# Optimization experiments

Hardware: AMD Instinct MI355X
Metric: run time of the kernel (lower is better)

The kernel has to match this reference:

```python
import jax, jax.numpy as jnp
import numpy as np

H = 16
N_TASKS, N_DATA, N_DEV = 400_000, 200_000, 8


def _edges(key, n_src, n_dst, e):
    k1, k2 = jax.random.split(key)
    src = jax.random.randint(k1, (e,), 0, n_src)
    dst = jax.random.randint(k2, (e,), 0, n_dst)
    return jnp.stack([src, dst]).astype(jnp.int64)


def setup_inputs() -> dict:
    key = jax.random.key(0)
    ks = jax.random.split(key, 16)
    inp = {
        "x_tasks": jax.random.normal(ks[0], (N_TASKS, 12), jnp.float32),
        "x_data": jax.random.normal(ks[1], (N_DATA, 5), jnp.float32),
        "x_devices": jax.random.normal(ks[2], (N_DEV, 12), jnp.float32),
        "ei_data_tasks": _edges(ks[3], N_DATA, N_TASKS, 1_600_000),
        "ei_tasks_data": _edges(ks[4], N_TASKS, N_DATA, 1_600_000),
        "ei_tasks_devices": _edges(ks[5], N_TASKS, N_DEV, 400_000),
        "ei_devices_tasks": _edges(ks[6], N_DEV, N_TASKS, 400_000),
        "ei_data_devices": _edges(ks[7], N_DATA, N_DEV, 200_000),
        "ei_devices_data": _edges(ks[8], N_DEV, N_DATA, 200_000),
        "ei_tt_to": _edges(ks[9], N_TASKS, N_TASKS, 800_000),
        "ei_tt_from": _edges(ks[10], N_TASKS, N_TASKS, 800_000),
        # stacked GraphConv weights, grouped by input dim
        # W_rel5:  [0]=data->tasks, [1]=data->devices
        "W_rel5": jax.random.normal(ks[11], (2, 5, H), jnp.float32) * 0.3,
        # W_rel12: [0]=tasks->data,[1]=tasks->devices,[2]=devices->tasks,[3]=devices->data,[4]=tt_to,[5]=tt_from
        "W_rel12": jax.random.normal(ks[12], (6, 12, H), jnp.float32) * 0.2,
        # b_rel order: dt_t, t_d, t_dev, dev_t, d_dev, dev_d, tt_to, tt_from
        "b_rel": jax.random.normal(ks[13], (8, H), jnp.float32) * 0.1,
        # W_root5: [0]=tasks->data (dst data), [1]=devices->data
        "W_root5": jax.random.normal(ks[14], (2, 5, H), jnp.float32) * 0.3,
        # W_root12: [0]=data->tasks,[1]=tasks->devices,[2]=devices->tasks,[3]=data->devices,[4]=tt_to,[5]=tt_from
        "W_root12": jax.random.normal(ks[15], (6, 12, H), jnp.float32) * 0.2,
        # LayerNorm params: [0]=tasks, [1]=data, [2]=devices
        "ln_gamma": jnp.ones((3, H), jnp.float32),
        "ln_beta": jnp.zeros((3, H), jnp.float32),
    }
    return inp


def _graph_conv(x_src, x_dst, ei, W_rel, b_rel, W_root):
    # PyG GraphConv(aggr='add'): lin_rel(scatter_add(x_src[src] -> dst)) + lin_root(x_dst)
    agg = jax.ops.segment_sum(x_src[ei[0]], ei[1], num_segments=x_dst.shape[0])
    return agg @ W_rel + b_rel + x_dst @ W_root


def _layer_norm(x, gamma, beta, eps=1e-5):
    mu = jnp.mean(x, axis=-1, keepdims=True)
    var = jnp.mean(jnp.square(x - mu), axis=-1, keepdims=True)
    return (x - mu) * jax.lax.rsqrt(var + eps) * gamma + beta


def reference(x_tasks, x_data, x_devices,
              ei_data_tasks, ei_tasks_data, ei_tasks_devices, ei_devices_tasks,
              ei_data_devices, ei_devices_data, ei_tt_to, ei_tt_from,
              W_rel5, W_rel12, b_rel, W_root5, W_root12, ln_gamma, ln_beta):
    # HeteroConv(aggr='sum'): sum relation outputs per destination node type
    tasks = (
        _graph_conv(x_data, x_tasks, ei_data_tasks, W_rel5[0], b_rel[0], W_root12[0])
        + _graph_conv(x_devices, x_tasks, ei_devices_tasks, W_rel12[2], b_rel[3], W_root12[2])
        + _graph_conv(x_tasks, x_tasks, ei_tt_to, W_rel12[4], b_rel[6], W_root12[4])
        + _graph_conv(x_tasks, x_tasks, ei_tt_from, W_rel12[5], b_rel[7], W_root12[5])
    )
    data = (
        _graph_conv(x_tasks, x_data, ei_tasks_data, W_rel12[0], b_rel[1], W_root5[0])
        + _graph_conv(x_devices, x_data, ei_devices_data, W_rel12[3], b_rel[5], W_root5[1])
    )
    devices = (
        _graph_conv(x_tasks, x_devices, ei_tasks_devices, W_rel12[1], b_rel[2], W_root12[1])
        + _graph_conv(x_data, x_devices, ei_data_devices, W_rel5[1], b_rel[4], W_root12[3])
    )
    slope = 0.01
    tasks = jax.nn.leaky_relu(_layer_norm(tasks, ln_gamma[0], ln_beta[0]), slope)
    data = jax.nn.leaky_relu(_layer_norm(data, ln_gamma[1], ln_beta[1]), slope)
    devices = jax.nn.leaky_relu(_layer_norm(devices, ln_gamma[2], ln_beta[2]), slope)
    return tasks, data, devices
```

## Files before the change

kernel.cpp:

```cpp
#include <hip/hip_runtime.h>
#include <hip/hip_fp16.h>

#define LRELU(v) ((v) >= 0.0f ? (v) : 0.01f * (v))
#define EPB 8192
#define SHIFT 7
#define PAIRS 1600

struct PartDesc {
    const int* src; const int* dst;
    unsigned* part; int* cursor;
    int E, B, cap, chunk0;
    unsigned tag;
};

struct PrepArgs {
    PartDesc r[6];
    int part_end;
    const int *tdev_e; int E_tdev; int sd12_b0, sd12_nb;
    const int *ddev_e; int E_ddev; int sd5_b0, sd5_nb;
    const float *x_tasks, *x_data, *x_dev;
    float *aggT_dev, *aggD_dev;
    __half *h_tasks; int NT; int ct_b0;
    __half *h_data;  int ND; int cd_b0;
};

template<int F>
__device__ __forceinline__ void loadrow(const float* __restrict__ x, unsigned s, float* v) {
    const float* p = x + (size_t)s * F;
    #pragma unroll
    for (int f = 0; f < F; ++f) v[f] = p[f];
}
template<>
__device__ __forceinline__ void loadrow<12>(const float* __restrict__ x, unsigned s, float* v) {
    const float4* p = (const float4*)(x + (size_t)s * 12);
    float4 a = p[0], b = p[1], c = p[2];
    v[0]=a.x; v[1]=a.y; v[2]=a.z; v[3]=a.w;
    v[4]=b.x; v[5]=b.y; v[6]=b.z; v[7]=b.w;
    v[8]=c.x; v[9]=c.y; v[10]=c.z; v[11]=c.w;
}

template<int F>
__device__ void scatter_dev_body(const float* __restrict__ x, const int* __restrict__ src,
                                 const int* __restrict__ dst, int E,
                                 float* __restrict__ agg, float* s_agg,
                                 int bl, int nb, int t)
{
    for (int i = t; i < 8 * F; i += 256) s_agg[i] = 0.0f;
    __syncthreads();
    const int stride = nb * 256;
    for (int e = bl * 256 + t; e < E; e += stride) {
        float v[F];
        loadrow<F>(x, (unsigned)src[e], v);
        int d = dst[e];
        #pragma unroll
        for (int f = 0; f < F; ++f) atomicAdd(&s_agg[d * F + f], v[f]);
    }
    __syncthreads();
    if (t < 8 * F) atomicAdd(&agg[t], s_agg[t]);
}

__global__ __launch_bounds__(256)
void prep_k(PrepArgs A)
{
    __shared__ unsigned shp[2 * PAIRS];
    const int bid = blockIdx.x;
    const int t = threadIdx.x;

    if (bid < A.part_end) {
        unsigned* hist = shp;
        unsigned* base = shp + PAIRS;
        int ri = 0;
        #pragma unroll
        for (int k = 1; k < 6; ++k) if (bid >= A.r[k].chunk0) ri = k;
        const PartDesc d = A.r[ri];
        const int e0 = (bid - d.chunk0) * EPB;
        const int e1 = min(d.E, e0 + EPB);
        const int npair = (d.B + 1) >> 1;

        for (int i = t; i < npair; i += 256) hist[i] = 0u;
        __syncthreads();
        for (int e = e0 + t; e < e1; e += 256) {
            int b = d.dst[e] >> SHIFT;
            atomicAdd(&hist[b >> 1], 1u << ((b & 1) << 4));
        }
        __syncthreads();
        for (int i = t; i < npair; i += 256) {
            unsigned h = hist[i];
            unsigned lo = h & 0xffffu, hi = h >> 16;
            unsigned blo = lo ? (unsigned)atomicAdd(&d.cursor[2 * i],     (int)lo) : 0u;
            unsigned bhi = hi ? (unsigned)atomicAdd(&d.cursor[2 * i + 1], (int)hi) : 0u;
            base[i] = (blo & 0xffffu) | (bhi << 16);
            hist[i] = 0u;
        }
        __syncthreads();
        for (int e = e0 + t; e < e1; e += 256) {
            int dd = d.dst[e];
            int b = dd >> SHIFT;
            unsigned s16 = (unsigned)(b & 1) << 4;
            unsigned r = atomicAdd(&hist[b >> 1], 1u << s16);
            unsigned idx = ((r >> s16) & 0xffffu) + ((base[b >> 1] >> s16) & 0xffffu);
            if ((int)idx < d.cap)
                d.part[(size_t)b * d.cap + idx] =
                    ((unsigned)d.src[e] << 9) | (((unsigned)dd & 127u) << 2) | d.tag;
        }
    } else if (bid < A.sd5_b0) {
        scatter_dev_body<12>(A.x_tasks, A.tdev_e, A.tdev_e + A.E_tdev, A.E_tdev,
                             A.aggT_dev, (float*)shp, bid - A.sd12_b0, A.sd12_nb, t);
    } else if (bid < A.ct_b0) {
        scatter_dev_body<5>(A.x_data, A.ddev_e, A.ddev_e + A.E_ddev, A.E_ddev,
                            A.aggD_dev, (float*)shp, bid - A.sd5_b0, A.sd5_nb, t);
    } else if (bid < A.cd_b0) {
        int row = (bid - A.ct_b0) * 256 + t;
        if (row < A.NT) {
            const float* xr = A.x_tasks + (size_t)row * 12;
            __half h[16];
            #pragma unroll
            for (int j = 0; j < 12; ++j) h[j] = __float2half(xr[j]);
            #pragma unroll
            for (int j = 12; j < 16; ++j) h[j] = __half(0.0f);
            uint4* dst = (uint4*)(A.h_tasks + (size_t)row * 16);
            dst[0] = *(const uint4*)h;
            dst[1] = *(const uint4*)(h + 8);
        }
    } else {
        int row = (bid - A.cd_b0) * 256 + t;
        if (row < A.ND) {
            const float* xr = A.x_data + (size_t)row * 5;
            __half h[8];
            #pragma unroll
            for (int j = 0; j < 5; ++j) h[j] = __float2half(xr[j]);
            #pragma unroll
            for (int j = 5; j < 8; ++j) h[j] = __half(0.0f);
            *(uint4*)(A.h_data + (size_t)row * 8) = *(const uint4*)h;
        }
    }
}

struct FusedArgs {
    const unsigned *p_task, *p_data;
    const int *c_task, *c_data;
    int cap_t, cap_d;
    const __half *h_tasks, *h_data;
    const float *x_dev, *x_tasks, *x_data;
    const float *aggT_dev, *aggD_dev;
    const float *W_rel5, *W_rel12, *b_rel, *W_root5, *W_root12, *ln_g, *ln_b;
    float *out_tasks, *out_data, *out_dev;
    int NT, ND, NDEV, Bt, Bd;
};

__device__ __forceinline__ void issue_task(unsigned e, const FusedArgs& A, uint4* r) {
    unsigned rel = e & 3u, s = e >> 9;
    if (rel == 0u) {
        r[0] = *(const uint4*)(A.h_data + (size_t)s * 8);
    } else if (rel == 1u) {
        const uint4* q = (const uint4*)(A.x_dev + (size_t)s * 12);
        r[0] = q[0]; r[1] = q[1]; r[2] = q[2];
    } else {
        const uint4* q = (const uint4*)(A.h_tasks + (size_t)s * 16);
        r[0] = q[0]; r[1] = q[1];
    }
}
__device__ __forceinline__ void commit_task(unsigned e, const uint4* r, float* acc) {
    unsigned rel = e & 3u;
    float* a = acc + ((e >> 2) & 127u) * 41;
    if (rel == 0u) {
        const __half2* h = (const __half2*)r;
        float2 f0 = __half22float2(h[0]), f1 = __half22float2(h[1]), f2 = __half22float2(h[2]);
        atomicAdd(a + 0, f0.x); atomicAdd(a + 1, f0.y);
        atomicAdd(a + 2, f1.x); atomicAdd(a + 3, f1.y);
        atomicAdd(a + 4, f2.x);
    } else if (rel == 1u) {
        const float* f = (const float*)r;
        #pragma unroll
        for (int j = 0; j < 12; ++j) atomicAdd(a + 5 + j, f[j]);
    } else {
        float* base = a + (rel == 2u ? 17 : 29);
        const __half2* h = (const __half2*)r;
        #pragma unroll
        for (int j = 0; j < 6; ++j) {
            float2 f = __half22float2(h[j]);
            atomicAdd(base + 2 * j,     f.x);
            atomicAdd(base + 2 * j + 1, f.y);
        }
    }
}

__device__ __forceinline__ void issue_data(unsigned e, const FusedArgs& A, uint4* r) {
    unsigned rel = e & 3u, s = e >> 9;
    if (rel == 0u) {
        const uint4* q = (const uint4*)(A.h_tasks + (size_t)s * 16);
        r[0] = q[0]; r[1] = q[1];
    } else {
        const uint4* q = (const uint4*)(A.x_dev + (size_t)s * 12);
        r[0] = q[0]; r[1] = q[1]; r[2] = q[2];
    }
}
__device__ __forceinline__ void commit_data(unsigned e, const uint4* r, float* acc) {
    unsigned rel = e & 3u;
    float* a = acc + ((e >> 2) & 127u) * 25;
    if (rel == 0u) {
        const __half2* h = (const __half2*)r;
        #pragma unroll
        for (int j = 0; j < 6; ++j) {
            float2 f = __half22float2(h[j]);
            atomicAdd(a + 2 * j,     f.x);
            atomicAdd(a + 2 * j + 1, f.y);
        }
    } else {
        const float* f = (const float*)r;
        #pragma unroll
        for (int j = 0; j < 12; ++j) atomicAdd(a + 12 + j, f[j]);
    }
}

__device__ __forceinline__
void ln_store(float* o, const float* __restrict__ sg, const float* __restrict__ sbt,
              float* __restrict__ op)
{
    float mu = 0.0f;
    #pragma unroll
    for (int k = 0; k < 16; ++k) mu += o[k];
    mu *= 0.0625f;
    float var = 0.0f;
    #pragma unroll
    for (int k = 0; k < 16; ++k) { float d = o[k] - mu; var = fmaf(d, d, var); }
    var *= 0.0625f;
    const float r = rsqrtf(var + 1e-5f);
    #pragma unroll
    for (int k = 0; k < 16; ++k) {
        float v = (o[k] - mu) * r * sg[k] + sbt[k];
        o[k] = LRELU(v);
    }
    float4* q = (float4*)op;
    const float4* s = (const float4*)o;
    q[0] = s[0]; q[1] = s[1]; q[2] = s[2]; q[3] = s[3];
}

__global__ __launch_bounds__(512, 8)
void fused_k(FusedArgs A)
{
    __shared__ __align__(16) float lds[6144];
    const int bid = blockIdx.x;
    const int t = threadIdx.x;

    if (bid < A.Bt) {
        float* acc = lds;
        float* sW  = lds + 5248;
        float* sb  = lds + 6096;
        float* sg  = lds + 6112;
        float* sbt = lds + 6128;

        for (int i = t; i < 5248; i += 512) acc[i] = 0.0f;
        for (int i = t; i < 80; i += 512) sW[i] = A.W_rel5[i];
        for (int i = t; i < 192; i += 512) {
            sW[80  + i] = A.W_rel12[384 + i];
            sW[272 + i] = A.W_rel12[768 + i];
            sW[464 + i] = A.W_rel12[960 + i];
            sW[656 + i] = A.W_root12[i] + A.W_root12[384 + i]
                        + A.W_root12[768 + i] + A.W_root12[960 + i];
        }
        if (t < 16) {
            sb[t]  = A.b_rel[t] + A.b_rel[48 + t] + A.b_rel[96 + t] + A.b_rel[112 + t];
            sg[t]  = A.ln_g[t];
            sbt[t] = A.ln_b[t];
        }
        __syncthreads();

        const unsigned* p = A.p_task + (size_t)bid * A.cap_t;
        const int cnt = min(A.c_task[bid], A.cap_t);
        int i = t;
        for (; i + 512 < cnt; i += 1024) {
            unsigned e0 = p[i], e1 = p[i + 512];
            uint4 r0[3], r1[3];
            issue_task(e0, A, r0);
            issue_task(e1, A, r1);
            commit_task(e0, r0, acc);
            commit_task(e1, r1, acc);
        }
        if (i < cnt) {
            unsigned e = p[i];
            uint4 r[3];
            issue_task(e, A, r);
            commit_task(e, r, acc);
        }
        __syncthreads();

        const int node = t >> 2, part = t & 3;
        const int row = (bid << SHIFT) + node;
        if (row < A.NT) {
            const float* ar = acc + node * 41;
            const int p4 = part * 4;
            float o0 = sb[p4], o1 = sb[p4 + 1], o2 = sb[p4 + 2], o3 = sb[p4 + 3];
            #pragma unroll
            for (int f = 0; f < 41; ++f) {
                float v = ar[f];
                float4 w = *(const float4*)(sW + f * 16 + p4);
                o0 = fmaf(v, w.x, o0); o1 = fmaf(v, w.y, o1);
                o2 = fmaf(v, w.z, o2); o3 = fmaf(v, w.w, o3);
            }
            const float* xr = A.x_tasks + (size_t)row * 12;
            #pragma unroll
            for (int f = 0; f < 12; ++f) {
                float v = xr[f];
                float4 w = *(const float4*)(sW + (41 + f) * 16 + p4);
                o0 = fmaf(v, w.x, o0); o1 = fmaf(v, w.y, o1);
                o2 = fmaf(v, w.z, o2); o3 = fmaf(v, w.w, o3);
            }
            float s = o0 + o1 + o2 + o3;
            s += __shfl_xor(s, 1); s += __shfl_xor(s, 2);
            const float mu = s * 0.0625f;
            float d0 = o0 - mu, d1 = o1 - mu, d2 = o2 - mu, d3 = o3 - mu;
            float q = d0*d0 + d1*d1 + d2*d2 + d3*d3;
            q += __shfl_xor(q, 1); q += __shfl_xor(q, 2);
            const float r = rsqrtf(q * 0.0625f + 1e-5f);
            float4 out;
            out.x = LRELU(d0 * r * sg[p4]     + sbt[p4]);
            out.y = LRELU(d1 * r * sg[p4 + 1] + sbt[p4 + 1]);
            out.z = LRELU(d2 * r * sg[p4 + 2] + sbt[p4 + 2]);
            out.w = LRELU(d3 * r * sg[p4 + 3] + sbt[p4 + 3]);
            *(float4*)(A.out_tasks + (size_t)row * 16 + p4) = out;
        }
    } else if (bid < A.Bt + A.Bd) {
        float* acc = lds;
        float* sW  = lds + 3200;
        float* sb  = lds + 3664;
        float* sg  = lds + 3680;
        float* sbt = lds + 3696;

        for (int i = t; i < 3200; i += 512) acc[i] = 0.0f;
        for (int i = t; i < 192; i += 512) {
            sW[i]       = A.W_rel12[i];
            sW[192 + i] = A.W_rel12[576 + i];
        }
        for (int i = t; i < 80; i += 512)
            sW[384 + i] = A.W_root5[i] + A.W_root5[80 + i];
        if (t < 16) {
            sb[t]  = A.b_rel[16 + t] + A.b_rel[80 + t];
            sg[t]  = A.ln_g[16 + t];
            sbt[t] = A.ln_b[16 + t];
        }
        __syncthreads();

        const int b = bid - A.Bt;
        const unsigned* p = A.p_data + (size_t)b * A.cap_d;
        const int cnt = min(A.c_data[b], A.cap_d);
        int i = t;
        for (; i + 512 < cnt; i += 1024) {
            unsigned e0 = p[i], e1 = p[i + 512];
            uint4 r0[3], r1[3];
            issue_data(e0, A, r0);
            issue_data(e1, A, r1);
            commit_data(e0, r0, acc);
            commit_data(e1, r1, acc);
        }
        if (i < cnt) {
            unsigned e = p[i];
            uint4 r[3];
            issue_data(e, A, r);
            commit_data(e, r, acc);
        }
        __syncthreads();

        const int node = t >> 2, part = t & 3;
        const int row = (b << SHIFT) + node;
        if (row < A.ND) {
            const float* ar = acc + node * 25;
            const int p4 = part * 4;
            float o0 = sb[p4], o1 = sb[p4 + 1], o2 = sb[p4 + 2], o3 = sb[p4 + 3];
            #pragma unroll
            for (int f = 0; f < 24; ++f) {
                float v = ar[f];
                float4 w = *(const float4*)(sW + f * 16 + p4);
                o0 = fmaf(v, w.x, o0); o1 = fmaf(v, w.y, o1);
                o2 = fmaf(v, w.z, o2); o3 = fmaf(v, w.w, o3);
            }
            const float* xr = A.x_data + (size_t)row * 5;
            #pragma unroll
            for (int f = 0; f < 5; ++f) {
                float v = xr[f];
                float4 w = *(const float4*)(sW + (24 + f) * 16 + p4);
                o0 = fmaf(v, w.x, o0); o1 = fmaf(v, w.y, o1);
                o2 = fmaf(v, w.z, o2); o3 = fmaf(v, w.w, o3);
            }
            float s = o0 + o1 + o2 + o3;
            s += __shfl_xor(s, 1); s += __shfl_xor(s, 2);
            const float mu = s * 0.0625f;
            float d0 = o0 - mu, d1 = o1 - mu, d2 = o2 - mu, d3 = o3 - mu;
            float q = d0*d0 + d1*d1 + d2*d2 + d3*d3;
            q += __shfl_xor(q, 1); q += __shfl_xor(q, 2);
            const float r = rsqrtf(q * 0.0625f + 1e-5f);
            float4 out;
            out.x = LRELU(d0 * r * sg[p4]     + sbt[p4]);
            out.y = LRELU(d1 * r * sg[p4 + 1] + sbt[p4 + 1]);
            out.z = LRELU(d2 * r * sg[p4 + 2] + sbt[p4 + 2]);
            out.w = LRELU(d3 * r * sg[p4 + 3] + sbt[p4 + 3]);
            *(float4*)(A.out_data + (size_t)row * 16 + p4) = out;
        }
    } else {
        const int i = t;
        if (i < A.NDEV) {
            float o[16];
            #pragma unroll
            for (int k = 0; k < 16; ++k) o[k] = A.b_rel[32 + k] + A.b_rel[64 + k];
            #pragma unroll
            for (int j = 0; j < 12; ++j) {
                float fj = A.aggT_dev[i * 12 + j];
                #pragma unroll
                for (int k = 0; k < 16; ++k) o[k] = fmaf(fj, A.W_rel12[192 + j * 16 + k], o[k]);
            }
            #pragma unroll
            for (int j = 0; j < 5; ++j) {
                float fj = A.aggD_dev[i * 5 + j];
                #pragma unroll
                for (int k = 0; k < 16; ++k) o[k] = fmaf(fj, A.W_rel5[80 + j * 16 + k], o[k]);
            }
            #pragma unroll
            for (int j = 0; j < 12; ++j) {
                float fj = A.x_dev[i * 12 + j];
                #pragma unroll
                for (int k = 0; k < 16; ++k)
                    o[k] = fmaf(fj, A.W_root12[192 + j * 16 + k] + A.W_root12[576 + j * 16 + k], o[k]);
            }
            ln_store(o, A.ln_g + 32, A.ln_b + 32, A.out_dev + (size_t)i * 16);
        }
    }
}

extern "C" void kernel_launch(void* const* d_in, const int* in_sizes, int n_in,
                              void* d_out, int out_size, void* d_ws, size_t ws_size,
                              hipStream_t stream)
{
    const float* x_tasks = (const float*)d_in[0];
    const float* x_data  = (const float*)d_in[1];
    const float* x_dev   = (const float*)d_in[2];
    const int* ei_dt    = (const int*)d_in[3];
    const int* ei_td    = (const int*)d_in[4];
    const int* ei_tdev  = (const int*)d_in[5];
    const int* ei_devt  = (const int*)d_in[6];
    const int* ei_ddev  = (const int*)d_in[7];
    const int* ei_devd  = (const int*)d_in[8];
    const int* ei_to    = (const int*)d_in[9];
    const int* ei_from  = (const int*)d_in[10];
    const float* W_rel5   = (const float*)d_in[11];
    const float* W_rel12  = (const float*)d_in[12];
    const float* b_rel    = (const float*)d_in[13];
    const float* W_root5  = (const float*)d_in[14];
    const float* W_root12 = (const float*)d_in[15];
    const float* ln_g     = (const float*)d_in[16];
    const float* ln_b     = (const float*)d_in[17];

    const int NT   = in_sizes[0] / 12;
    const int ND   = in_sizes[1] / 5;
    const int NDEV = in_sizes[2] / 12;
    const int E_dt   = in_sizes[3]  / 2;
    const int E_td   = in_sizes[4]  / 2;
    const int E_tdev = in_sizes[5]  / 2;
    const int E_devt = in_sizes[6]  / 2;
    const int E_ddev = in_sizes[7]  / 2;
    const int E_devd = in_sizes[8]  / 2;
    const int E_to   = in_sizes[9]  / 2;
    const int E_from = in_sizes[10] / 2;

    const int B_t = (NT + 127) / 128;
    const int B_d = (ND + 127) / 128;

    auto capf = [](long long E, int B) {
        int mean = (int)(E / B) + 1;
        int c = mean + mean / 4 + 128;
        return (c + 3) & ~3;
    };
    const int cap_t = capf((long long)E_dt + E_devt + E_to + E_from, B_t);
    const int cap_d = capf((long long)E_td + E_devd, B_d);

    float* ws = (float*)d_ws;
    size_t o = 0;
    int* c_task = (int*)(ws + o); o += 3200;
    int* c_data = (int*)(ws + o); o += 1600;
    float* aggT_dev = ws + o; o += 96;
    float* aggD_dev = ws + o; o += 48;
    const size_t zero_bytes = o * sizeof(float);
    o = (o + 3) & ~(size_t)3;
    __half* h_tasks = (__half*)(ws + o); o += (size_t)NT * 8;
    __half* h_data  = (__half*)(ws + o); o += (size_t)ND * 4;
    unsigned* p_task = (unsigned*)(ws + o); o += (size_t)B_t * cap_t;
    unsigned* p_data = (unsigned*)(ws + o); o += (size_t)B_d * cap_d;

    hipMemsetAsync(d_ws, 0, zero_bytes, stream);

    auto nc = [](int e) { return (e + EPB - 1) / EPB; };
    PrepArgs pa;
    int ch = 0;
    pa.r[0] = { ei_dt,   ei_dt   + E_dt,   p_task, c_task, E_dt,   B_t, cap_t, ch, 0u }; ch += nc(E_dt);
    pa.r[1] = { ei_devt, ei_devt + E_devt, p_task, c_task, E_devt, B_t, cap_t, ch, 1u }; ch += nc(E_devt);
    pa.r[2] = { ei_to,   ei_to   + E_to,   p_task, c_task, E_to,   B_t, cap_t, ch, 2u }; ch += nc(E_to);
    pa.r[3] = { ei_from, ei_from + E_from, p_task, c_task, E_from, B_t, cap_t, ch, 3u }; ch += nc(E_from);
    pa.r[4] = { ei_td,   ei_td   + E_td,   p_data, c_data, E_td,   B_d, cap_d, ch, 0u }; ch += nc(E_td);
    pa.r[5] = { ei_devd, ei_devd + E_devd, p_data, c_data, E_devd, B_d, cap_d, ch, 1u }; ch += nc(E_devd);
    pa.part_end = ch;
    pa.tdev_e = ei_tdev; pa.E_tdev = E_tdev; pa.sd12_b0 = ch; pa.sd12_nb = 192; ch += 192;
    pa.ddev_e = ei_ddev; pa.E_ddev = E_ddev; pa.sd5_b0  = ch; pa.sd5_nb  = 96;  ch += 96;
    pa.x_tasks = x_tasks; pa.x_data = x_data; pa.x_dev = x_dev;
    pa.aggT_dev = aggT_dev; pa.aggD_dev = aggD_dev;
    pa.h_tasks = h_tasks; pa.NT = NT; pa.ct_b0 = ch; ch += (NT + 255) / 256;
    pa.h_data  = h_data;  pa.ND = ND; pa.cd_b0 = ch; ch += (ND + 255) / 256;

    prep_k<<<ch, 256, 0, stream>>>(pa);

    float* out_tasks = (float*)d_out;
    float* out_data  = out_tasks + (size_t)NT * 16;
    float* out_dev   = out_data  + (size_t)ND * 16;

    FusedArgs fa;
    fa.p_task = p_task; fa.p_data = p_data;
    fa.c_task = c_task; fa.c_data = c_data;
    fa.cap_t = cap_t; fa.cap_d = cap_d;
    fa.h_tasks = h_tasks; fa.h_data = h_data;
    fa.x_dev = x_dev; fa.x_tasks = x_tasks; fa.x_data = x_data;
    fa.aggT_dev = aggT_dev; fa.aggD_dev = aggD_dev;
    fa.W_rel5 = W_rel5; fa.W_rel12 = W_rel12; fa.b_rel = b_rel;
    fa.W_root5 = W_root5; fa.W_root12 = W_root12; fa.ln_g = ln_g; fa.ln_b = ln_b;
    fa.out_tasks = out_tasks; fa.out_data = out_data; fa.out_dev = out_dev;
    fa.NT = NT; fa.ND = ND; fa.NDEV = NDEV;
    fa.Bt = B_t; fa.Bd = B_d;

    fused_k<<<B_t + B_d + 1, 512, 0, stream>>>(fa);
}
```

Baseline: 597.9 us.

## Split prep kernel into partition and misc kernels with larger chunks

Splits the single multi-role prep kernel into a partitioning kernel that uses 512 threads and 16384 edges per block, and a separate kernel that handles device scatter and fp16 conversion with a small shared buffer. The aim is to lift occupancy for the misc blocks, which no longer reserve the partition's large shared histogram, and to halve the number of global cursor atomics by using bigger chunks. It also hoists the root-feature row loads ahead of the FMA loops in the finalize code. The cost is an extra kernel launch. Larger chunks also give fewer partition blocks and may risk the 16-bit per-bucket counter limit.

```diff
diff --git a/kernel.cpp b/kernel.cpp
--- a/kernel.cpp
+++ b/kernel.cpp
@@ -2,7 +2,7 @@
 #include <hip/hip_fp16.h>
 
 #define LRELU(v) ((v) >= 0.0f ? (v) : 0.01f * (v))
-#define EPB 8192
+#define EPB 16384
 #define SHIFT 7
 #define PAIRS 1600
 
@@ -13,9 +13,56 @@
     unsigned tag;
 };
 
-struct PrepArgs {
+struct PartArgs {
     PartDesc r[6];
-    int part_end;
+};
+
+__global__ __launch_bounds__(512)
+void prep_part_k(PartArgs A)
+{
+    __shared__ unsigned shp[2 * PAIRS];
+    const int bid = blockIdx.x;
+    const int t = threadIdx.x;
+
+    unsigned* hist = shp;
+    unsigned* base = shp + PAIRS;
+    int ri = 0;
+    #pragma unroll
+    for (int k = 1; k < 6; ++k) if (bid >= A.r[k].chunk0) ri = k;
+    const PartDesc d = A.r[ri];
+    const int e0 = (bid - d.chunk0) * EPB;
+    const int e1 = min(d.E, e0 + EPB);
+    const int npair = (d.B + 1) >> 1;
+
+    for (int i = t; i < npair; i += 512) hist[i] = 0u;
+    __syncthreads();
+    for (int e = e0 + t; e < e1; e += 512) {
+        int b = d.dst[e] >> SHIFT;
+        atomicAdd(&hist[b >> 1], 1u << ((b & 1) << 4));
+    }
+    __syncthreads();
+    for (int i = t; i < npair; i += 512) {
+        unsigned h = hist[i];
+        unsigned lo = h & 0xffffu, hi = h >> 16;
+        unsigned blo = lo ? (unsigned)atomicAdd(&d.cursor[2 * i],     (int)lo) : 0u;
+        unsigned bhi = hi ? (unsigned)atomicAdd(&d.cursor[2 * i + 1], (int)hi) : 0u;
+        base[i] = (blo & 0xffffu) | (bhi << 16);
+        hist[i] = 0u;
+    }
+    __syncthreads();
+    for (int e = e0 + t; e < e1; e += 512) {
+        int dd = d.dst[e];
+        int b = dd >> SHIFT;
+        unsigned s16 = (unsigned)(b & 1) << 4;
+        unsigned r = atomicAdd(&hist[b >> 1], 1u << s16);
+        unsigned idx = ((r >> s16) & 0xffffu) + ((base[b >> 1] >> s16) & 0xffffu);
+        if ((int)idx < d.cap)
+            d.part[(size_t)b * d.cap + idx] =
+                ((unsigned)d.src[e] << 9) | (((unsigned)dd & 127u) << 2) | d.tag;
+    }
+}
+
+struct MiscArgs {
     const int *tdev_e; int E_tdev; int sd12_b0, sd12_nb;
     const int *ddev_e; int E_ddev; int sd5_b0, sd5_nb;
     const float *x_tasks, *x_data, *x_dev;
@@ -60,55 +107,18 @@
 }
 
 __global__ __launch_bounds__(256)
-void prep_k(PrepArgs A)
+void prep_misc_k(MiscArgs A)
 {
-    __shared__ unsigned shp[2 * PAIRS];
+    __shared__ float s_agg[96];
     const int bid = blockIdx.x;
     const int t = threadIdx.x;
 
-    if (bid < A.part_end) {
-        unsigned* hist = shp;
-        unsigned* base = shp + PAIRS;
-        int ri = 0;
-        #pragma unroll
-        for (int k = 1; k < 6; ++k) if (bid >= A.r[k].chunk0) ri = k;
-        const PartDesc d = A.r[ri];
-        const int e0 = (bid - d.chunk0) * EPB;
-        const int e1 = min(d.E, e0 + EPB);
-        const int npair = (d.B + 1) >> 1;
-
-        for (int i = t; i < npair; i += 256) hist[i] = 0u;
-        __syncthreads();
-        for (int e = e0 + t; e < e1; e += 256) {
-            int b = d.dst[e] >> SHIFT;
-            atomicAdd(&hist[b >> 1], 1u << ((b & 1) << 4));
-        }
-        __syncthreads();
-        for (int i = t; i < npair; i += 256) {
-            unsigned h = hist[i];
-            unsigned lo = h & 0xffffu, hi = h >> 16;
-            unsigned blo = lo ? (unsigned)atomicAdd(&d.cursor[2 * i],     (int)lo) : 0u;
-            unsigned bhi = hi ? (unsigned)atomicAdd(&d.cursor[2 * i + 1], (int)hi) : 0u;
-            base[i] = (blo & 0xffffu) | (bhi << 16);
-            hist[i] = 0u;
-        }
-        __syncthreads();
-        for (int e = e0 + t; e < e1; e += 256) {
-            int dd = d.dst[e];
-            int b = dd >> SHIFT;
-            unsigned s16 = (unsigned)(b & 1) << 4;
-            unsigned r = atomicAdd(&hist[b >> 1], 1u << s16);
-            unsigned idx = ((r >> s16) & 0xffffu) + ((base[b >> 1] >> s16) & 0xffffu);
-            if ((int)idx < d.cap)
-                d.part[(size_t)b * d.cap + idx] =
-                    ((unsigned)d.src[e] << 9) | (((unsigned)dd & 127u) << 2) | d.tag;
-        }
-    } else if (bid < A.sd5_b0) {
+    if (bid < A.sd5_b0) {
         scatter_dev_body<12>(A.x_tasks, A.tdev_e, A.tdev_e + A.E_tdev, A.E_tdev,
-                             A.aggT_dev, (float*)shp, bid - A.sd12_b0, A.sd12_nb, t);
+                             A.aggT_dev, s_agg, bid - A.sd12_b0, A.sd12_nb, t);
     } else if (bid < A.ct_b0) {
         scatter_dev_body<5>(A.x_data, A.ddev_e, A.ddev_e + A.E_ddev, A.E_ddev,
-                            A.aggD_dev, (float*)shp, bid - A.sd5_b0, A.sd5_nb, t);
+                            A.aggD_dev, s_agg, bid - A.sd5_b0, A.sd5_nb, t);
     } else if (bid < A.cd_b0) {
         int row = (bid - A.ct_b0) * 256 + t;
         if (row < A.NT) {
@@ -290,6 +300,8 @@
         if (row < A.NT) {
             const float* ar = acc + node * 41;
             const int p4 = part * 4;
+            const float4* xr = (const float4*)(A.x_tasks + (size_t)row * 12);
+            float4 x0 = xr[0], x1 = xr[1], x2 = xr[2];
             float o0 = sb[p4], o1 = sb[p4 + 1], o2 = sb[p4 + 2], o3 = sb[p4 + 3];
             #pragma unroll
             for (int f = 0; f < 41; ++f) {
@@ -298,10 +310,10 @@
                 o0 = fmaf(v, w.x, o0); o1 = fmaf(v, w.y, o1);
                 o2 = fmaf(v, w.z, o2); o3 = fmaf(v, w.w, o3);
             }
-            const float* xr = A.x_tasks + (size_t)row * 12;
+            float xf[12] = {x0.x,x0.y,x0.z,x0.w, x1.x,x1.y,x1.z,x1.w, x2.x,x2.y,x2.z,x2.w};
             #pragma unroll
             for (int f = 0; f < 12; ++f) {
-                float v = xr[f];
+                float v = xf[f];
                 float4 w = *(const float4*)(sW + (41 + f) * 16 + p4);
                 o0 = fmaf(v, w.x, o0); o1 = fmaf(v, w.y, o1);
                 o2 = fmaf(v, w.z, o2); o3 = fmaf(v, w.w, o3);
@@ -366,6 +378,7 @@
         if (row < A.ND) {
             const float* ar = acc + node * 25;
             const int p4 = part * 4;
+            const float* xr = A.x_data + (size_t)row * 5;
             float o0 = sb[p4], o1 = sb[p4 + 1], o2 = sb[p4 + 2], o3 = sb[p4 + 3];
             #pragma unroll
             for (int f = 0; f < 24; ++f) {
@@ -374,7 +387,6 @@
                 o0 = fmaf(v, w.x, o0); o1 = fmaf(v, w.y, o1);
                 o2 = fmaf(v, w.z, o2); o3 = fmaf(v, w.w, o3);
             }
-            const float* xr = A.x_data + (size_t)row * 5;
             #pragma unroll
             for (int f = 0; f < 5; ++f) {
                 float v = xr[f];
@@ -488,7 +500,7 @@
     hipMemsetAsync(d_ws, 0, zero_bytes, stream);
 
     auto nc = [](int e) { return (e + EPB - 1) / EPB; };
-    PrepArgs pa;
+    PartArgs pa;
     int ch = 0;
     pa.r[0] = { ei_dt,   ei_dt   + E_dt,   p_task, c_task, E_dt,   B_t, cap_t, ch, 0u }; ch += nc(E_dt);
     pa.r[1] = { ei_devt, ei_devt + E_devt, p_task, c_task, E_devt, B_t, cap_t, ch, 1u }; ch += nc(E_devt);
@@ -496,15 +508,19 @@
     pa.r[3] = { ei_from, ei_from + E_from, p_task, c_task, E_from, B_t, cap_t, ch, 3u }; ch += nc(E_from);
     pa.r[4] = { ei_td,   ei_td   + E_td,   p_data, c_data, E_td,   B_d, cap_d, ch, 0u }; ch += nc(E_td);
     pa.r[5] = { ei_devd, ei_devd + E_devd, p_data, c_data, E_devd, B_d, cap_d, ch, 1u }; ch += nc(E_devd);
-    pa.part_end = ch;
-    pa.tdev_e = ei_tdev; pa.E_tdev = E_tdev; pa.sd12_b0 = ch; pa.sd12_nb = 192; ch += 192;
-    pa.ddev_e = ei_ddev; pa.E_ddev = E_ddev; pa.sd5_b0  = ch; pa.sd5_nb  = 96;  ch += 96;
-    pa.x_tasks = x_tasks; pa.x_data = x_data; pa.x_dev = x_dev;
-    pa.aggT_dev = aggT_dev; pa.aggD_dev = aggD_dev;
-    pa.h_tasks = h_tasks; pa.NT = NT; pa.ct_b0 = ch; ch += (NT + 255) / 256;
-    pa.h_data  = h_data;  pa.ND = ND; pa.cd_b0 = ch; ch += (ND + 255) / 256;
-
-    prep_k<<<ch, 256, 0, stream>>>(pa);
+
+    prep_part_k<<<ch, 512, 0, stream>>>(pa);
+
+    MiscArgs ma;
+    int mb = 0;
+    ma.tdev_e = ei_tdev; ma.E_tdev = E_tdev; ma.sd12_b0 = mb; ma.sd12_nb = 192; mb += 192;
+    ma.ddev_e = ei_ddev; ma.E_ddev = E_ddev; ma.sd5_b0  = mb; ma.sd5_nb  = 96;  mb += 96;
+    ma.x_tasks = x_tasks; ma.x_data = x_data; ma.x_dev = x_dev;
+    ma.aggT_dev = aggT_dev; ma.aggD_dev = aggD_dev;
+    ma.h_tasks = h_tasks; ma.NT = NT; ma.ct_b0 = mb; mb += (NT + 255) / 256;
+    ma.h_data  = h_data;  ma.ND = ND; ma.cd_b0 = mb; mb += (ND + 255) / 256;
+
+    prep_misc_k<<<mb, 256, 0, stream>>>(ma);
 
     float* out_tasks = (float*)d_out;
     float* out_data  = out_tasks + (size_t)NT * 16;
```

Result: slower. 621.0 us (+3.9%).
